# Kernel optimization log

Hardware: AMD Instinct MI355X
Metric: run time of the kernel (lower is better)

## Reference

```python
import jax, jax.numpy as jnp
import numpy as np

DEV_VDW, VDW_N, MAXV, MINV, DM_MIN = 0.2, 6.0, 0.0356, 0.0178, 0.5


def setup_inputs() -> dict:
    key = jax.random.key(0)
    ks = iter(jax.random.split(key, 64))
    B, N1, N2, D, L = 8, 128, 256, 128, 3
    f = jnp.float32
    nrm = lambda shape, s=0.05: jax.random.normal(next(ks), shape, f) * s
    ligand_h = jax.random.normal(next(ks), (B, N1, 54), f)
    target_h = jax.random.normal(next(ks), (B, N2, 54), f)
    def adj(n):
        a = (jax.random.uniform(next(ks), (B, n, n)) < 0.08).astype(f)
        a = jnp.maximum(a, jnp.swapaxes(a, 1, 2))
        return jnp.maximum(a, jnp.eye(n, dtype=f))
    ligand_adj = adj(N1)
    target_adj = adj(N2)
    interaction_indice = jax.random.uniform(next(ks), (B, 3, N1, N2), f)
    ligand_pos = jax.random.normal(next(ks), (B, N1, 3), f) * 2.0
    target_pos = jax.random.normal(next(ks), (B, N2, 3), f) * 4.0
    rotor = jax.random.uniform(next(ks), (B,), f) * 10.0
    ligand_vdw_radii = 1.2 + 0.8 * jax.random.uniform(next(ks), (B, N1), f)
    target_vdw_radii = 1.2 + 0.8 * jax.random.uniform(next(ks), (B, N2), f)
    return dict(
        ligand_h=ligand_h, ligand_adj=ligand_adj, target_h=target_h, target_adj=target_adj,
        interaction_indice=interaction_indice, ligand_pos=ligand_pos, target_pos=target_pos,
        rotor=rotor, ligand_vdw_radii=ligand_vdw_radii, target_vdw_radii=target_vdw_radii,
        ligand_valid=jnp.ones((B, N1), f), target_valid=jnp.ones((B, N2), f),
        ligand_non_metal=jnp.ones((B, N1), f), target_non_metal=jnp.ones((B, N2), f),
        emb_w=nrm((54, D)),
        gat_w=nrm((L, D, D)), gat_b=jnp.zeros((L, D), f), gat_att=nrm((L, D, D)),
        gat_gate_w=nrm((L, 2 * D, 1)), gat_gate_b=jnp.zeros((L, 1), f),
        int_wt_w=nrm((L, D, D)), int_wt_b=jnp.zeros((L, D), f),
        int_mt_w=nrm((L, D, D)), int_mt_b=jnp.zeros((L, D), f),
        gru_w_ih=nrm((L, 3 * D, D)), gru_w_hh=nrm((L, 3 * D, D)),
        gru_b_ih=jnp.zeros((L, 3 * D), f), gru_b_hh=jnp.zeros((L, 3 * D), f),
        A_w1=nrm((2 * D, D)), A_b1=jnp.zeros((D,), f), A_w2=nrm((D, 1)), A_b2=jnp.zeros((1,), f),
        B_w1=nrm((2 * D, D)), B_b1=jnp.zeros((D,), f), B_w2=nrm((D, 1)), B_b2=jnp.zeros((1,), f),
        hbond_coeff=jnp.array([1.0], f), hydrophobic_coeff=jnp.array([0.5], f),
        rotor_coeff=jnp.array([0.5], f),
    )


def reference(ligand_h, ligand_adj, target_h, target_adj, interaction_indice, ligand_pos,
              target_pos, rotor, ligand_vdw_radii, target_vdw_radii, ligand_valid,
              target_valid, ligand_non_metal, target_non_metal, emb_w, gat_w, gat_b,
              gat_att, gat_gate_w, gat_gate_b, int_wt_w, int_wt_b, int_mt_w, int_mt_b,
              gru_w_ih, gru_w_hh, gru_b_ih, gru_b_hh, A_w1, A_b1, A_w2, A_b2, B_w1, B_b1,
              B_w2, B_b2, hbond_coeff, hydrophobic_coeff, rotor_coeff):
    B, D, L = ligand_h.shape[0], emb_w.shape[1], gat_w.shape[0]

    def dist(lpos):
        diff = lpos[:, :, None, :] - target_pos[:, None, :, :]
        dm = jnp.sqrt((diff * diff).sum(-1) + 1e-10)
        return jnp.where(dm < DM_MIN, 1e10, dm)

    dm = dist(ligand_pos)

    def gat(x, adj, i):
        nt = x @ gat_w[i] + gat_b[i]                                   # [B,N,D]
        ea = jnp.einsum('bjl,bkl->bjk', nt @ gat_att[i], nt)
        ea = ea + jnp.swapaxes(ea, 1, 2)
        aw = jax.nn.softmax(jnp.where(adj > 1e-6, ea, -9e15), axis=-1) * adj
        out = jax.nn.relu(jnp.einsum('bij,bjd->bid', aw, nt))
        gate = jax.nn.sigmoid(jnp.concatenate([x, out], -1) @ gat_gate_w[i] + gat_gate_b[i])
        return gate * x + (1.0 - gate) * out

    lh = ligand_h @ emb_w
    th = target_h @ emb_w
    for i in range(L):
        lh = gat(lh, ligand_adj, i)
        th = gat(th, target_adj, i)

    adj12 = jax.lax.stop_gradient(dm)
    adj12 = jnp.where(adj12 > 5.0, 0.0, adj12)
    adj12 = jnp.where(adj12 > 1e-3, 1.0, 0.0)
    adj21 = jnp.swapaxes(adj12, 1, 2)

    def inter(a1, a2, ev, i):
        t1 = a1 @ int_wt_w[i] + int_wt_b[i]
        m2 = a2 @ int_mt_w[i] + int_mt_b[i]                            # [B,N2,D]
        t2 = (m2[:, None, :, :] * ev[..., None]).max(axis=2)           # [B,N1,D]
        msg = jax.nn.relu(t1 + t2)
        gi = msg @ gru_w_ih[i].T + gru_b_ih[i]
        gh = a1 @ gru_w_hh[i].T + gru_b_hh[i]
        i_r, i_z, i_n = jnp.split(gi, 3, -1)
        h_r, h_z, h_n = jnp.split(gh, 3, -1)
        r = jax.nn.sigmoid(i_r + h_r)
        z = jax.nn.sigmoid(i_z + h_z)
        n = jnp.tanh(i_n + r * h_n)
        return (1.0 - z) * n + z * a1

    for i in range(L):
        lh, th = inter(lh, th, adj12, i), inter(th, lh, adj21, i)

    N1, N2 = lh.shape[1], th.shape[1]
    h_cat = jnp.concatenate([
        jnp.broadcast_to(lh[:, :, None, :], (B, N1, N2, D)),
        jnp.broadcast_to(th[:, None, :, :], (B, N1, N2, D))], -1)      # [B,N1,N2,2D]

    A_raw = jax.nn.sigmoid(jax.nn.relu(h_cat @ A_w1 + A_b1) @ A_w2 + A_b2)[..., 0]
    B_raw = jnp.tanh(jax.nn.relu(h_cat @ B_w1 + B_b1) @ B_w2 + B_b2)[..., 0] * DEV_VDW
    dm0 = ligand_vdw_radii[:, :, None] + target_vdw_radii[:, None, :] + B_raw
    valid_pair = ligand_non_metal[:, :, None] * target_non_metal[:, None, :]
    A_vdw = A_raw * (MAXV - MINV) + MINV

    def energies_of(dm):
        dm0c = jnp.where(dm0 < 1e-4, 1.0, dm0)
        r6 = (dm0c / dm) ** VDW_N
        evdw = A_vdw * (jnp.minimum(r6 * r6 - 2.0 * r6, 100.0) * valid_pair)
        vdw_val = evdw.sum((1, 2))[:, None]
        dmd = dm - dm0
        def hb(Aind):
            r = jnp.clip(dmd * Aind / -0.7, 0.0, 1.0) * -(hbond_coeff[0] * hbond_coeff[0])
            return r.sum((1, 2))[:, None]
        hbond = hb(interaction_indice[:, 0])
        metal = hb(interaction_indice[:, 1])
        hp = jnp.clip((-dmd + 1.5) * interaction_indice[:, 2], 0.0, 1.0)
        hp = hp * -(hydrophobic_coeff[0] * hydrophobic_coeff[0])
        e = jnp.concatenate([vdw_val, hbond, metal, hp.sum((1, 2))[:, None]], -1)
        return e / (1.0 + rotor_coeff[0] * rotor_coeff[0] * rotor[:, None])

    energies = energies_of(dm)
    esum = lambda p: energies_of(dist(p)).sum()
    g = jax.grad(esum)(ligand_pos)
    der1 = (g.sum(1) ** 2).mean()
    der2 = -jax.grad(lambda p: jax.grad(esum)(p).sum())(ligand_pos).sum((1, 2)).mean()
    return energies, der1, der2
```

## Files before the change

kernel.cpp:

```cpp
#include <hip/hip_runtime.h>
#include <math.h>

#define BB 8
#define N1C 128
#define N2C 256
#define DC 128
#define NHC 54
#define ROWS_L 1024
#define ROWS_T 2048
#define ROWS_ALL 3072

__device__ __forceinline__ float wredSum(float v) {
#pragma unroll
  for (int o = 32; o > 0; o >>= 1) v += __shfl_down(v, o);
  return v;
}
__device__ float blockSum(float v) {
  __shared__ float red[9];
  v = wredSum(v);
  int lane = threadIdx.x & 63, wid = threadIdx.x >> 6;
  __syncthreads();
  if (lane == 0) red[wid] = v;
  __syncthreads();
  if (threadIdx.x == 0) {
    float s = 0.f;
    int nw = (blockDim.x + 63) >> 6;
    for (int i = 0; i < nw; ++i) s += red[i];
    red[8] = s;
  }
  __syncthreads();
  return red[8];
}

__global__ __launch_bounds__(256) void k_prep(
    const float* __restrict__ LP, const float* __restrict__ TP,
    float* __restrict__ AD, const float* __restrict__ LH,
    const float* __restrict__ TH, const float* __restrict__ EW,
    float* __restrict__ H0, const float* __restrict__ GWp,
    const float* __restrict__ GBp, const float* __restrict__ ATT,
    float* __restrict__ WA, float* __restrict__ bA,
    const float* __restrict__ IH, const float* __restrict__ HH,
    float* __restrict__ GIHT, float* __restrict__ GHHT) {
  int bid = blockIdx.x, tid = threadIdx.x;
  if (bid < 1024) {
    long idx = (long)bid * 256 + tid;
    int j = idx & (N2C - 1);
    long t = idx >> 8;
    int i = (int)(t & (N1C - 1));
    int b = (int)(t >> 7);
    float dx = LP[((long)b * N1C + i) * 3 + 0] - TP[((long)b * N2C + j) * 3 + 0];
    float dy = LP[((long)b * N1C + i) * 3 + 1] - TP[((long)b * N2C + j) * 3 + 1];
    float dz = LP[((long)b * N1C + i) * 3 + 2] - TP[((long)b * N2C + j) * 3 + 2];
    float d = sqrtf(dx * dx + dy * dy + dz * dz + 1e-10f);
    if (d < 0.5f) d = 1e10f;
    AD[idx] = (d <= 5.0f && d > 1e-3f) ? 1.f : 0.f;
  } else if (bid < 1024 + 384) {
    int r0 = (bid - 1024) * 8;
    __shared__ float xs[8][NHC];
    for (int t = tid; t < 8 * NHC; t += 256) {
      int rr = r0 + t / NHC, c = t % NHC;
      xs[t / NHC][c] = (rr < ROWS_L) ? LH[(long)rr * NHC + c]
                                     : TH[(long)(rr - ROWS_L) * NHC + c];
    }
    __syncthreads();
    int d = tid & 127, rb = (tid >> 7) * 4;
    float a[4] = {0.f, 0.f, 0.f, 0.f};
#pragma unroll 6
    for (int k = 0; k < NHC; ++k) {
      float wv = EW[(long)k * DC + d];
#pragma unroll
      for (int r = 0; r < 4; ++r) a[r] += xs[rb + r][k] * wv;
    }
#pragma unroll
    for (int r = 0; r < 4; ++r) H0[(long)(r0 + rb + r) * DC + d] = a[r];
  } else if (bid < 1024 + 384 + 99) {
    int q = bid - 1408;
    int l = q / 33, bx = q % 33;
    const float* Wl = GWp + (long)l * DC * DC;
    const float* Al = ATT + (long)l * DC * DC;
    if (bx == 32) {
      if (tid < 128) {
        float acc = 0.f;
#pragma unroll 8
        for (int m = 0; m < DC; ++m)
          acc += GBp[l * DC + m] * Al[(long)m * DC + tid];
        bA[l * DC + tid] = acc;
      }
    } else {
      __shared__ float xs2[4][DC];
      int r0 = bx * 4;
      for (int t = tid; t < 4 * DC; t += 256)
        xs2[t >> 7][t & 127] = Wl[(long)r0 * DC + t];
      __syncthreads();
      if (tid < 128) {
        int d = tid;
        float a0 = 0.f, a1 = 0.f, a2 = 0.f, a3 = 0.f;
#pragma unroll 8
        for (int m = 0; m < DC; ++m) {
          float av = Al[(long)m * DC + d];
          a0 += xs2[0][m] * av;
          a1 += xs2[1][m] * av;
          a2 += xs2[2][m] * av;
          a3 += xs2[3][m] * av;
        }
        float* out = WA + (long)l * DC * DC + (long)r0 * DC + d;
        out[0] = a0;
        out[DC] = a1;
        out[2 * DC] = a2;
        out[3 * DC] = a3;
      }
    }
  } else {
    long idx = (long)(bid - 1507) * 256 + tid;
    if (idx < 6L * 49152) {
      int a = (int)(idx / 49152);
      int rem = (int)(idx % 49152);
      int l = a >> 1, whh = a & 1;
      int c = rem / 384, rr = rem % 384;
      const float* src = (whh ? HH : IH) + (long)l * 49152;
      float* dst = (whh ? GHHT : GIHT) + (long)l * 49152;
      dst[(long)c * 384 + rr] = src[(long)rr * 128 + c];
    }
  }
}

__global__ __launch_bounds__(256) void k_lin2h(
    const float* __restrict__ X, const float* __restrict__ W1,
    const float* __restrict__ b1, const float* __restrict__ W2,
    const float* __restrict__ b2, float* __restrict__ Y1, float* __restrict__ Y2,
    int rpb, int trans) {
  int r0 = blockIdx.x * 4;
  __shared__ float xs_t[DC][4];
  int tid = threadIdx.x;
  for (int t = tid; t < 4 * DC; t += 256) {
    int r = t >> 7, c = t & 127;
    xs_t[c][r] = X[(long)(r0 + r) * DC + c];
  }
  __syncthreads();
  int h = tid >> 7, d = tid & 127;
  const float* W = h ? W2 : W1;
  const float* bp = h ? b2 : b1;
  float* Y = h ? Y2 : Y1;
  float a0 = 0.f, a1 = 0.f, a2 = 0.f, a3 = 0.f;
#pragma unroll 8
  for (int k = 0; k < DC; ++k) {
    float4 xv = *(const float4*)&xs_t[k][0];
    float wv = W[(long)k * DC + d];
    a0 = fmaf(xv.x, wv, a0);
    a1 = fmaf(xv.y, wv, a1);
    a2 = fmaf(xv.z, wv, a2);
    a3 = fmaf(xv.w, wv, a3);
  }
  float bv = bp ? bp[d] : 0.f;
  float v[4] = {a0 + bv, a1 + bv, a2 + bv, a3 + bv};
  if (!trans) {
#pragma unroll
    for (int r = 0; r < 4; ++r) Y[(long)(r0 + r) * DC + d] = v[r];
  } else {
    int b = r0 / rpb, rin = r0 - b * rpb;
#pragma unroll
    for (int r = 0; r < 4; ++r)
      Y[((long)b * DC + d) * rpb + rin + r] = v[r];
  }
}

__global__ __launch_bounds__(256) void k_ea2(const float* __restrict__ NTp,
                                             const float* __restrict__ E1p,
                                             const float* __restrict__ ADJL,
                                             const float* __restrict__ ADJT,
                                             float* __restrict__ EAL,
                                             float* __restrict__ EAT) {
  int id = blockIdx.x;
  int N, base, j0, k0, b;
  const float* ADJ;
  float* EA;
  if (id < 64) {
    b = id >> 3;
    int rem = id & 7;
    N = N1C;
    base = b * N1C;
    j0 = (rem >> 1) * 32;
    k0 = (rem & 1) * 64;
    ADJ = ADJL + (long)b * N1C * N1C;
    EA = EAL + (long)b * N1C * N1C;
  } else {
    int q = id - 64;
    b = q >> 5;
    int rem = q & 31;
    N = N2C;
    base = ROWS_L + b * N2C;
    j0 = (rem >> 2) * 32;
    k0 = (rem & 3) * 64;
    ADJ = ADJT + (long)b * N2C * N2C;
    EA = EAT + (long)b * N2C * N2C;
  }
  __shared__ float aj_e1[32][34], aj_nt[32][34];
  __shared__ float bk_e1[32][68], bk_nt[32][68];
  int tid = threadIdx.x, tx = tid & 15, ty = tid >> 4;
  float acc[2][4];
#pragma unroll
  for (int r = 0; r < 2; ++r)
#pragma unroll
    for (int c = 0; c < 4; ++c) acc[r][c] = 0.f;
  for (int kc = 0; kc < DC; kc += 32) {
    __syncthreads();
    for (int t = tid; t < 1024; t += 256) {
      int kk = t & 31, rr = t >> 5;
      aj_e1[kk][rr] = E1p[(long)(base + j0 + rr) * DC + kc + kk];
      aj_nt[kk][rr] = NTp[(long)(base + j0 + rr) * DC + kc + kk];
    }
    for (int t = tid; t < 2048; t += 256) {
      int kk = t & 31, cc = t >> 5;
      bk_e1[kk][cc] = E1p[(long)(base + k0 + cc) * DC + kc + kk];
      bk_nt[kk][cc] = NTp[(long)(base + k0 + cc) * DC + kc + kk];
    }
    __syncthreads();
#pragma unroll
    for (int kk = 0; kk < 32; ++kk) {
      float2 ae = *(const float2*)&aj_e1[kk][ty * 2];
      float2 an = *(const float2*)&aj_nt[kk][ty * 2];
      float4 bn = *(const float4*)&bk_nt[kk][tx * 4];
      float4 be = *(const float4*)&bk_e1[kk][tx * 4];
      acc[0][0] = fmaf(ae.x, bn.x, fmaf(an.x, be.x, acc[0][0]));
      acc[0][1] = fmaf(ae.x, bn.y, fmaf(an.x, be.y, acc[0][1]));
      acc[0][2] = fmaf(ae.x, bn.z, fmaf(an.x, be.z, acc[0][2]));
      acc[0][3] = fmaf(ae.x, bn.w, fmaf(an.x, be.w, acc[0][3]));
      acc[1][0] = fmaf(ae.y, bn.x, fmaf(an.y, be.x, acc[1][0]));
      acc[1][1] = fmaf(ae.y, bn.y, fmaf(an.y, be.y, acc[1][1]));
      acc[1][2] = fmaf(ae.y, bn.z, fmaf(an.y, be.z, acc[1][2]));
      acc[1][3] = fmaf(ae.y, bn.w, fmaf(an.y, be.w, acc[1][3]));
    }
  }
#pragma unroll
  for (int r = 0; r < 2; ++r) {
    long rowi = (long)(j0 + ty * 2 + r) * N + k0 + tx * 4;
    float4 ad = *(const float4*)&ADJ[rowi];
    float4 o;
    o.x = (ad.x > 1e-6f) ? acc[r][0] : -9e15f;
    o.y = (ad.y > 1e-6f) ? acc[r][1] : -9e15f;
    o.z = (ad.z > 1e-6f) ? acc[r][2] : -9e15f;
    o.w = (ad.w > 1e-6f) ? acc[r][3] : -9e15f;
    *(float4*)&EA[rowi] = o;
  }
}

__global__ __launch_bounds__(512) void k_smagg(
    const float* __restrict__ EAL, const float* __restrict__ EAT,
    const float* __restrict__ NTp, const float* __restrict__ Xp,
    const float* __restrict__ GW, const float* __restrict__ GB,
    float* __restrict__ Y) {
  int z = blockIdx.z;
  int N = z ? N2C : N1C;
  if (blockIdx.x * 8 >= N) return;
  int ls = z ? 8 : 7;
  int baseRow = z ? ROWS_L : 0;
  const float* EA = z ? EAT : EAL;
  int b = blockIdx.y, i0 = blockIdx.x * 8;
  __shared__ float ps[8][N2C + 4];
  __shared__ float col[32][DC + 4];
  __shared__ float red[8][2];
  int tid = threadIdx.x;
  const float* EAb = EA + (long)b * N * N + (long)i0 * N;
  for (int t = tid; t < 8 * N; t += 512)
    ps[t >> ls][t & (N - 1)] = EAb[t];
  __syncthreads();
  {
    int r = tid >> 6, l = tid & 63;
    float m = -INFINITY;
    for (int k = l; k < N; k += 64) m = fmaxf(m, ps[r][k]);
#pragma unroll
    for (int o = 32; o > 0; o >>= 1) m = fmaxf(m, __shfl_xor(m, o));
    float s = 0.f;
    for (int k = l; k < N; k += 64) {
      float p = expf(ps[r][k] - m);
      ps[r][k] = p;
      s += p;
    }
#pragma unroll
    for (int o = 32; o > 0; o >>= 1) s += __shfl_xor(s, o);
    float inv = 1.f / s;
    for (int k = l; k < N; k += 64) ps[r][k] *= inv;
  }
  int d = tid & 127, ro = tid >> 7;
  float acc[2] = {0.f, 0.f};
  const float* NTb = NTp + (long)(baseRow + b * N) * DC;
  for (int k0 = 0; k0 < N; k0 += 32) {
    __syncthreads();
    for (int t = tid; t < 32 * DC; t += 512)
      col[t >> 7][t & 127] = NTb[(long)(k0 + (t >> 7)) * DC + (t & 127)];
    __syncthreads();
#pragma unroll 8
    for (int kk = 0; kk < 32; ++kk) {
      float cv = col[kk][d];
      acc[0] = fmaf(ps[ro][k0 + kk], cv, acc[0]);
      acc[1] = fmaf(ps[ro + 4][k0 + kk], cv, acc[1]);
    }
  }
  float gwd = GW[d], gwo = GW[DC + d];
  float xv[2], ov[2], part[2];
#pragma unroll
  for (int q = 0; q < 2; ++q) {
    int r = ro + 4 * q;
    float o = fmaxf(acc[q], 0.f);
    ov[q] = o;
    float x = Xp[(long)(baseRow + b * N + i0 + r) * DC + d];
    xv[q] = x;
    part[q] = x * gwd + o * gwo;
  }
  int wid = tid >> 6;
#pragma unroll
  for (int q = 0; q < 2; ++q) {
    float v = wredSum(part[q]);
    if ((tid & 63) == 0) red[wid][q] = v;
  }
  __syncthreads();
  float gb = GB[0];
#pragma unroll
  for (int q = 0; q < 2; ++q) {
    int r = ro + 4 * q;
    float s = red[2 * ro][q] + red[2 * ro + 1][q];
    float g = 1.f / (1.f + expf(-(s + gb)));
    Y[(long)(baseRow + b * N + i0 + r) * DC + d] = g * xv[q] + (1.f - g) * ov[q];
  }
}

__global__ __launch_bounds__(256) void k_msg2v(const float* __restrict__ T1,
                                               const float* __restrict__ M2,
                                               const float* __restrict__ EV,
                                               float* __restrict__ MSG) {
  int z = blockIdx.z, b = blockIdx.y;
  int Ni = z ? N2C : N1C, Nj = z ? N1C : N2C;
  if (blockIdx.x * 8 >= Ni) return;
  int t1off = z ? ROWS_L : 0, m2off = z ? 0 : ROWS_L;
  long ev_is = z ? 1L : (long)N2C, ev_js = z ? (long)N2C : 1L;
  int i0 = blockIdx.x * 8;
  __shared__ float m2s[32][DC + 4];
  __shared__ float evs[8][36];
  int dgrp = threadIdx.x & 31, row = threadIdx.x >> 5;
  int d0 = dgrp * 4;
  float a0 = -INFINITY, a1 = -INFINITY, a2 = -INFINITY, a3 = -INFINITY;
  const float* M2b = M2 + (long)(m2off + b * Nj) * DC;
  const float* EVb = EV + (long)b * (N1C * N2C);
  for (int j0 = 0; j0 < Nj; j0 += 32) {
    __syncthreads();
    for (int t = threadIdx.x; t < 32 * DC; t += 256)
      m2s[t >> 7][t & 127] = M2b[(long)(j0 + (t >> 7)) * DC + (t & 127)];
    for (int t = threadIdx.x; t < 256; t += 256)
      evs[t >> 5][t & 31] =
          EVb[(long)(i0 + (t >> 5)) * ev_is + (long)(j0 + (t & 31)) * ev_js];
    __syncthreads();
#pragma unroll 8
    for (int jj = 0; jj < 32; ++jj) {
      float4 m4 = *(const float4*)&m2s[jj][d0];
      float e = evs[row][jj];
      a0 = fmaxf(a0, m4.x * e);
      a1 = fmaxf(a1, m4.y * e);
      a2 = fmaxf(a2, m4.z * e);
      a3 = fmaxf(a3, m4.w * e);
    }
  }
  long grow = t1off + (long)b * Ni + i0 + row;
  float4 t4 = *(const float4*)&T1[grow * DC + d0];
  float4 o;
  o.x = fmaxf(t4.x + a0, 0.f);
  o.y = fmaxf(t4.y + a1, 0.f);
  o.z = fmaxf(t4.z + a2, 0.f);
  o.w = fmaxf(t4.w + a3, 0.f);
  *(float4*)&MSG[grow * DC + d0] = o;
}

__global__ __launch_bounds__(384) void k_gruf(
    const float* __restrict__ MSGp, const float* __restrict__ Hp,
    const float* __restrict__ WihT, const float* __restrict__ WhhT,
    const float* __restrict__ bih, const float* __restrict__ bhh,
    float* __restrict__ Y) {
  const int D = DC;
  int r0 = blockIdx.x * 4;
  __shared__ float xs_t[DC][4], hs_t[DC][4];
  __shared__ float gis[4][384], ghs[4][384];
  int tid = threadIdx.x;
  for (int t = tid; t < 4 * DC; t += 384) {
    int r = t >> 7, c = t & 127;
    xs_t[c][r] = MSGp[(long)(r0 + r) * D + c];
    hs_t[c][r] = Hp[(long)(r0 + r) * D + c];
  }
  __syncthreads();
  int dd = tid;
  float ai[4] = {0.f, 0.f, 0.f, 0.f}, ah[4] = {0.f, 0.f, 0.f, 0.f};
#pragma unroll 8
  for (int k = 0; k < DC; ++k) {
    float4 xv = *reinterpret_cast<const float4*>(&xs_t[k][0]);
    float4 hv = *reinterpret_cast<const float4*>(&hs_t[k][0]);
    float wi = WihT[(long)k * 384 + dd];
    float wh = WhhT[(long)k * 384 + dd];
    ai[0] = fmaf(xv.x, wi, ai[0]);
    ai[1] = fmaf(xv.y, wi, ai[1]);
    ai[2] = fmaf(xv.z, wi, ai[2]);
    ai[3] = fmaf(xv.w, wi, ai[3]);
    ah[0] = fmaf(hv.x, wh, ah[0]);
    ah[1] = fmaf(hv.y, wh, ah[1]);
    ah[2] = fmaf(hv.z, wh, ah[2]);
    ah[3] = fmaf(hv.w, wh, ah[3]);
  }
  float bi = bih[dd], bh = bhh[dd];
#pragma unroll
  for (int r = 0; r < 4; ++r) {
    gis[r][dd] = ai[r] + bi;
    ghs[r][dd] = ah[r] + bh;
  }
  __syncthreads();
  for (int t = tid; t < 4 * DC; t += 384) {
    int r = t >> 7, d = t & 127;
    float ir = gis[r][d], iz = gis[r][d + 128], inn = gis[r][d + 256];
    float hr = ghs[r][d], hz = ghs[r][d + 128], hn = ghs[r][d + 256];
    float rg = 1.f / (1.f + expf(-(ir + hr)));
    float zg = 1.f / (1.f + expf(-(iz + hz)));
    float ng = tanhf(inn + rg * hn);
    Y[(long)(r0 + r) * D + d] = (1.f - zg) * ng + zg * hs_t[d][r];
  }
}

__global__ __launch_bounds__(256) void k_pair(
    const float* __restrict__ UA, const float* __restrict__ VAT,
    const float* __restrict__ UB, const float* __restrict__ VBT,
    const float* __restrict__ AW2, const float* __restrict__ AB2,
    const float* __restrict__ BW2, const float* __restrict__ BB2,
    const float* __restrict__ LP, const float* __restrict__ TP,
    const float* __restrict__ LVDW, const float* __restrict__ TVDW,
    const float* __restrict__ LNM, const float* __restrict__ TNM,
    const float* __restrict__ II, const float* __restrict__ HBC,
    const float* __restrict__ HPC, float* __restrict__ PART) {
  const int D = DC, N1 = N1C, N2 = N2C;
  int i = blockIdx.x, b = blockIdx.y, j = threadIdx.x;
  __shared__ float ua[128], ub[128], wa2[128], wb2[128];
  if (j < 128) {
    long rb = ((long)b * N1 + i) * D + j;
    ua[j] = UA[rb];
    ub[j] = UB[rb];
    wa2[j] = AW2[j];
    wb2[j] = BW2[j];
  }
  __syncthreads();
  const float* vat = VAT + (long)b * D * N2;
  const float* vbt = VBT + (long)b * D * N2;
  float dotA = 0.f, dotB = 0.f;
#pragma unroll 8
  for (int d = 0; d < D; ++d) {
    dotA += fmaxf(ua[d] + vat[(long)d * N2 + j], 0.f) * wa2[d];
    dotB += fmaxf(ub[d] + vbt[(long)d * N2 + j], 0.f) * wb2[d];
  }
  float A_raw = 1.f / (1.f + expf(-(dotA + AB2[0])));
  float A_vdw = A_raw * (0.0356f - 0.0178f) + 0.0178f;
  float B_raw = tanhf(dotB + BB2[0]) * 0.2f;

  float lx = LP[((long)b * N1 + i) * 3 + 0];
  float ly = LP[((long)b * N1 + i) * 3 + 1];
  float lz = LP[((long)b * N1 + i) * 3 + 2];
  float tx = TP[((long)b * N2 + j) * 3 + 0];
  float ty = TP[((long)b * N2 + j) * 3 + 1];
  float tz = TP[((long)b * N2 + j) * 3 + 2];
  float dx = lx - tx, dy = ly - ty, dz = lz - tz;
  float s2 = dx * dx + dy * dy + dz * dz + 1e-10f;
  float draw = sqrtf(s2);
  bool clamped = draw < 0.5f;
  float dmv = clamped ? 1e10f : draw;

  float dm0 = LVDW[b * N1 + i] + TVDW[b * N2 + j] + B_raw;
  float dm0c = (dm0 < 1e-4f) ? 1.f : dm0;
  float valid = LNM[b * N1 + i] * TNM[b * N2 + j];

  float rr = dm0c / dmv;
  float r2 = rr * rr, r6 = r2 * r2 * r2;
  float fv = r6 * r6 - 2.f * r6;
  float evdw = A_vdw * (fminf(fv, 100.f) * valid);

  float dmd = dmv - dm0;
  long ii0 = ((long)b * 3) * N1 * N2 + (long)i * N2 + j;
  float I0 = II[ii0];
  float I1 = II[ii0 + (long)N1 * N2];
  float I2 = II[ii0 + 2L * N1 * N2];
  float hb2 = HBC[0] * HBC[0], hp2 = HPC[0] * HPC[0];
  float u0 = dmd * I0 / (-0.7f);
  float u1 = dmd * I1 / (-0.7f);
  float vv = (1.5f - dmd) * I2;
  float ehb = fminf(fmaxf(u0, 0.f), 1.f) * (-hb2);
  float emt = fminf(fmaxf(u1, 0.f), 1.f) * (-hb2);
  float ehp = fminf(fmaxf(vv, 0.f), 1.f) * (-hp2);

  float gx = 0.f, gy = 0.f, gz = 0.f, d2t = 0.f;
  if (!clamped) {
    float Ep = 0.f, Epp = 0.f;
    if (fv < 100.f) {
      float c = A_vdw * valid;
      Ep += c * (-12.f) * r6 * (r6 - 1.f) / draw;
      Epp += c * r6 * (156.f * r6 - 84.f) / s2;
    }
    if (u0 > 0.f && u0 < 1.f) Ep += hb2 * I0 * (1.f / 0.7f);
    if (u1 > 0.f && u1 < 1.f) Ep += hb2 * I1 * (1.f / 0.7f);
    if (vv > 0.f && vv < 1.f) Ep += hp2 * I2;
    float invd = 1.f / draw;
    gx = Ep * dx * invd;
    gy = Ep * dy * invd;
    gz = Ep * dz * invd;
    float T = dx + dy + dz;
    float tt = T * T / s2;
    d2t = Epp * tt + Ep * (3.f - tt) * invd;
  }

  float o0 = blockSum(evdw);
  float o1 = blockSum(ehb);
  float o2 = blockSum(emt);
  float o3 = blockSum(ehp);
  float o4 = blockSum(gx);
  float o5 = blockSum(gy);
  float o6 = blockSum(gz);
  float o7 = blockSum(d2t);
  if (j == 0) {
    float* p = PART + ((long)b * N1 + i) * 8;
    p[0] = o0; p[1] = o1; p[2] = o2; p[3] = o3;
    p[4] = o4; p[5] = o5; p[6] = o6; p[7] = o7;
  }
}

__global__ void k_final(const float* __restrict__ PART, const float* __restrict__ ROT,
                        const float* __restrict__ RC, float* __restrict__ OUT) {
  const int N1 = N1C;
  __shared__ float s[8][8];
  int t = threadIdx.x;
  if (t < 64) {
    int b = t >> 3, k1 = t & 7;
    float acc = 0.f;
    for (int i = 0; i < N1; ++i) acc += PART[((long)b * N1 + i) * 8 + k1];
    s[b][k1] = acc;
  }
  __syncthreads();
  if (t == 0) {
    float rcc = RC[0] * RC[0];
    float der1 = 0.f, der2 = 0.f;
    for (int b = 0; b < 8; ++b) {
      float w = 1.f / (1.f + rcc * ROT[b]);
      OUT[b * 4 + 0] = s[b][0] * w;
      OUT[b * 4 + 1] = s[b][1] * w;
      OUT[b * 4 + 2] = s[b][2] * w;
      OUT[b * 4 + 3] = s[b][3] * w;
      for (int c = 0; c < 3; ++c) {
        float S = s[b][4 + c] * w;
        der1 += S * S;
      }
      der2 += s[b][7] * w;
    }
    OUT[32] = der1 / 24.f;
    OUT[33] = -der2 / 8.f;
  }
}

extern "C" void kernel_launch(void* const* d_in, const int* in_sizes, int n_in,
                              void* d_out, int out_size, void* d_ws, size_t ws_size,
                              hipStream_t stream) {
  (void)in_sizes; (void)n_in; (void)out_size; (void)ws_size;
  const int D = DC;

  const float* ligand_h   = (const float*)d_in[0];
  const float* ligand_adj = (const float*)d_in[1];
  const float* target_h   = (const float*)d_in[2];
  const float* target_adj = (const float*)d_in[3];
  const float* inter_ind  = (const float*)d_in[4];
  const float* ligand_pos = (const float*)d_in[5];
  const float* target_pos = (const float*)d_in[6];
  const float* rotor      = (const float*)d_in[7];
  const float* lvdw       = (const float*)d_in[8];
  const float* tvdw       = (const float*)d_in[9];
  const float* lnm        = (const float*)d_in[12];
  const float* tnm        = (const float*)d_in[13];
  const float* emb_w      = (const float*)d_in[14];
  const float* gat_w      = (const float*)d_in[15];
  const float* gat_b      = (const float*)d_in[16];
  const float* gat_att    = (const float*)d_in[17];
  const float* gat_gate_w = (const float*)d_in[18];
  const float* gat_gate_b = (const float*)d_in[19];
  const float* int_wt_w   = (const float*)d_in[20];
  const float* int_wt_b   = (const float*)d_in[21];
  const float* int_mt_w   = (const float*)d_in[22];
  const float* int_mt_b   = (const float*)d_in[23];
  const float* gru_w_ih   = (const float*)d_in[24];
  const float* gru_w_hh   = (const float*)d_in[25];
  const float* gru_b_ih   = (const float*)d_in[26];
  const float* gru_b_hh   = (const float*)d_in[27];
  const float* A_w1       = (const float*)d_in[28];
  const float* A_b1       = (const float*)d_in[29];
  const float* A_w2       = (const float*)d_in[30];
  const float* A_b2       = (const float*)d_in[31];
  const float* B_w1       = (const float*)d_in[32];
  const float* B_b1       = (const float*)d_in[33];
  const float* B_w2       = (const float*)d_in[34];
  const float* B_b2       = (const float*)d_in[35];
  const float* hb_c       = (const float*)d_in[36];
  const float* hp_c       = (const float*)d_in[37];
  const float* rc_c       = (const float*)d_in[38];

  float* w = (float*)d_ws;
  auto take = [&](size_t n) { float* p = w; w += n; return p; };
  float* H0    = take((size_t)ROWS_ALL * DC);
  float* H1    = take((size_t)ROWS_ALL * DC);
  float* NT    = take((size_t)ROWS_ALL * DC);
  float* E1    = take((size_t)ROWS_ALL * DC);
  float* EAL   = take((size_t)BB * N1C * N1C);
  float* EAT   = take((size_t)BB * N2C * N2C);
  float* ADJ12 = take((size_t)BB * N1C * N2C);
  float* WA    = take((size_t)3 * DC * DC);
  float* bA    = take((size_t)3 * DC);
  float* GIHT  = take((size_t)3 * DC * 384);
  float* GHHT  = take((size_t)3 * DC * 384);
  float* PART  = take((size_t)BB * N1C * 8);
  float* T1  = NT;
  float* M2  = E1;
  float* MSG = EAT;
  float* UA  = EAL;
  float* UB  = EAT;
  float* VAT = NT;
  float* VBT = E1;

  k_prep<<<2659, 256, 0, stream>>>(ligand_pos, target_pos, ADJ12, ligand_h,
                                   target_h, emb_w, H0, gat_w, gat_b, gat_att,
                                   WA, bA, gru_w_ih, gru_w_hh, GIHT, GHHT);

  float *cur = H0, *alt = H1;

  for (int l = 0; l < 3; ++l) {
    k_lin2h<<<ROWS_ALL / 4, 256, 0, stream>>>(
        cur, gat_w + (size_t)l * D * D, gat_b + l * D, WA + (size_t)l * D * D,
        bA + l * D, NT, E1, 1, 0);
    k_ea2<<<320, 256, 0, stream>>>(NT, E1, ligand_adj, target_adj, EAL, EAT);
    k_smagg<<<dim3(N2C / 8, BB, 2), 512, 0, stream>>>(
        EAL, EAT, NT, cur, gat_gate_w + l * 2 * D, gat_gate_b + l, alt);
    float* t = cur; cur = alt; alt = t;
  }

  for (int l = 0; l < 3; ++l) {
    k_lin2h<<<ROWS_ALL / 4, 256, 0, stream>>>(
        cur, int_wt_w + (size_t)l * D * D, int_wt_b + l * D,
        int_mt_w + (size_t)l * D * D, int_mt_b + l * D, T1, M2, 1, 0);
    k_msg2v<<<dim3(32, 8, 2), 256, 0, stream>>>(T1, M2, ADJ12, MSG);
    k_gruf<<<ROWS_ALL / 4, 384, 0, stream>>>(MSG, cur, GIHT + (size_t)l * D * 384,
                                             GHHT + (size_t)l * D * 384,
                                             gru_b_ih + l * 384,
                                             gru_b_hh + l * 384, alt);
    float* t = cur; cur = alt; alt = t;
  }

  k_lin2h<<<ROWS_L / 4, 256, 0, stream>>>(cur, A_w1, A_b1, B_w1, B_b1, UA, UB,
                                          1, 0);
  k_lin2h<<<ROWS_T / 4, 256, 0, stream>>>(cur + (size_t)ROWS_L * DC,
                                          A_w1 + D * D, nullptr, B_w1 + D * D,
                                          nullptr, VAT, VBT, N2C, 1);

  k_pair<<<dim3(N1C, BB), 256, 0, stream>>>(UA, VAT, UB, VBT, A_w2, A_b2, B_w2,
                                            B_b2, ligand_pos, target_pos, lvdw,
                                            tvdw, lnm, tnm, inter_ind, hb_c,
                                            hp_c, PART);

  k_final<<<1, 256, 0, stream>>>(PART, rotor, rc_c, (float*)d_out);
}
```

Before: 351.2 us.

## Process more rows per block in smagg, GRU and pair kernels for reuse

Three kernels now do more rows per block so each staged operand is reused more. k_smagg handles 16 rows per block instead of 8, uses a 32-lane group per row, vectorises the column reads as float4 and reduces the gate within each group. k_gruf computes 8 rows per block so each weight load feeds 8 FMAs instead of 4. k_pair handles two ligand atoms per block, sharing the VAT/VBT column loads across both. The trade-offs are fewer blocks (lower occupancy and parallelism) and more registers per thread.

```diff
diff --git a/kernel.cpp b/kernel.cpp
--- a/kernel.cpp
+++ b/kernel.cpp
@@ -244,45 +244,45 @@
   }
 }
 
-__global__ __launch_bounds__(512) void k_smagg(
+__global__ __launch_bounds__(512) void k_smagg3(
     const float* __restrict__ EAL, const float* __restrict__ EAT,
     const float* __restrict__ NTp, const float* __restrict__ Xp,
     const float* __restrict__ GW, const float* __restrict__ GB,
     float* __restrict__ Y) {
   int z = blockIdx.z;
   int N = z ? N2C : N1C;
-  if (blockIdx.x * 8 >= N) return;
+  if (blockIdx.x * 16 >= N) return;
   int ls = z ? 8 : 7;
   int baseRow = z ? ROWS_L : 0;
   const float* EA = z ? EAT : EAL;
-  int b = blockIdx.y, i0 = blockIdx.x * 8;
-  __shared__ float ps[8][N2C + 4];
+  int b = blockIdx.y, i0 = blockIdx.x * 16;
+  __shared__ float ps[16][N2C + 4];
   __shared__ float col[32][DC + 4];
-  __shared__ float red[8][2];
+  __shared__ float red[16];
   int tid = threadIdx.x;
   const float* EAb = EA + (long)b * N * N + (long)i0 * N;
-  for (int t = tid; t < 8 * N; t += 512)
+  for (int t = tid; t < 16 * N; t += 512)
     ps[t >> ls][t & (N - 1)] = EAb[t];
   __syncthreads();
+  int r = tid >> 5, l = tid & 31;
   {
-    int r = tid >> 6, l = tid & 63;
     float m = -INFINITY;
-    for (int k = l; k < N; k += 64) m = fmaxf(m, ps[r][k]);
-#pragma unroll
-    for (int o = 32; o > 0; o >>= 1) m = fmaxf(m, __shfl_xor(m, o));
+    for (int k = l; k < N; k += 32) m = fmaxf(m, ps[r][k]);
+#pragma unroll
+    for (int o = 16; o > 0; o >>= 1) m = fmaxf(m, __shfl_xor(m, o));
     float s = 0.f;
-    for (int k = l; k < N; k += 64) {
+    for (int k = l; k < N; k += 32) {
       float p = expf(ps[r][k] - m);
       ps[r][k] = p;
       s += p;
     }
 #pragma unroll
-    for (int o = 32; o > 0; o >>= 1) s += __shfl_xor(s, o);
+    for (int o = 16; o > 0; o >>= 1) s += __shfl_xor(s, o);
     float inv = 1.f / s;
-    for (int k = l; k < N; k += 64) ps[r][k] *= inv;
-  }
-  int d = tid & 127, ro = tid >> 7;
-  float acc[2] = {0.f, 0.f};
+    for (int k = l; k < N; k += 32) ps[r][k] *= inv;
+  }
+  int d0 = l * 4;
+  float a0 = 0.f, a1 = 0.f, a2 = 0.f, a3 = 0.f;
   const float* NTb = NTp + (long)(baseRow + b * N) * DC;
   for (int k0 = 0; k0 < N; k0 += 32) {
     __syncthreads();
@@ -291,37 +291,32 @@
     __syncthreads();
 #pragma unroll 8
     for (int kk = 0; kk < 32; ++kk) {
-      float cv = col[kk][d];
-      acc[0] = fmaf(ps[ro][k0 + kk], cv, acc[0]);
-      acc[1] = fmaf(ps[ro + 4][k0 + kk], cv, acc[1]);
-    }
-  }
-  float gwd = GW[d], gwo = GW[DC + d];
-  float xv[2], ov[2], part[2];
-#pragma unroll
-  for (int q = 0; q < 2; ++q) {
-    int r = ro + 4 * q;
-    float o = fmaxf(acc[q], 0.f);
-    ov[q] = o;
-    float x = Xp[(long)(baseRow + b * N + i0 + r) * DC + d];
-    xv[q] = x;
-    part[q] = x * gwd + o * gwo;
-  }
-  int wid = tid >> 6;
-#pragma unroll
-  for (int q = 0; q < 2; ++q) {
-    float v = wredSum(part[q]);
-    if ((tid & 63) == 0) red[wid][q] = v;
-  }
-  __syncthreads();
-  float gb = GB[0];
-#pragma unroll
-  for (int q = 0; q < 2; ++q) {
-    int r = ro + 4 * q;
-    float s = red[2 * ro][q] + red[2 * ro + 1][q];
-    float g = 1.f / (1.f + expf(-(s + gb)));
-    Y[(long)(baseRow + b * N + i0 + r) * DC + d] = g * xv[q] + (1.f - g) * ov[q];
-  }
+      float4 c4 = *(const float4*)&col[kk][d0];
+      float p = ps[r][k0 + kk];
+      a0 = fmaf(p, c4.x, a0);
+      a1 = fmaf(p, c4.y, a1);
+      a2 = fmaf(p, c4.z, a2);
+      a3 = fmaf(p, c4.w, a3);
+    }
+  }
+  float4 gwd = *(const float4*)&GW[d0];
+  float4 gwo = *(const float4*)&GW[DC + d0];
+  float4 x4 = *(const float4*)&Xp[(long)(baseRow + b * N + i0 + r) * DC + d0];
+  float o0 = fmaxf(a0, 0.f), o1 = fmaxf(a1, 0.f);
+  float o2 = fmaxf(a2, 0.f), o3 = fmaxf(a3, 0.f);
+  float part = x4.x * gwd.x + o0 * gwo.x + x4.y * gwd.y + o1 * gwo.y +
+               x4.z * gwd.z + o2 * gwo.z + x4.w * gwd.w + o3 * gwo.w;
+#pragma unroll
+  for (int o = 16; o > 0; o >>= 1) part += __shfl_xor(part, o);
+  if (l == 0) red[r] = part;
+  __syncthreads();
+  float g = 1.f / (1.f + expf(-(red[r] + GB[0])));
+  float4 y;
+  y.x = g * x4.x + (1.f - g) * o0;
+  y.y = g * x4.y + (1.f - g) * o1;
+  y.z = g * x4.z + (1.f - g) * o2;
+  y.w = g * x4.w + (1.f - g) * o3;
+  *(float4*)&Y[(long)(baseRow + b * N + i0 + r) * DC + d0] = y;
 }
 
 __global__ __launch_bounds__(256) void k_msg2v(const float* __restrict__ T1,
@@ -375,41 +370,53 @@
     const float* __restrict__ bih, const float* __restrict__ bhh,
     float* __restrict__ Y) {
   const int D = DC;
-  int r0 = blockIdx.x * 4;
-  __shared__ float xs_t[DC][4], hs_t[DC][4];
-  __shared__ float gis[4][384], ghs[4][384];
+  int r0 = blockIdx.x * 8;
+  __shared__ float xs_t[DC][8], hs_t[DC][8];
+  __shared__ float gis[8][384], ghs[8][384];
   int tid = threadIdx.x;
-  for (int t = tid; t < 4 * DC; t += 384) {
+  for (int t = tid; t < 8 * DC; t += 384) {
     int r = t >> 7, c = t & 127;
     xs_t[c][r] = MSGp[(long)(r0 + r) * D + c];
     hs_t[c][r] = Hp[(long)(r0 + r) * D + c];
   }
   __syncthreads();
   int dd = tid;
-  float ai[4] = {0.f, 0.f, 0.f, 0.f}, ah[4] = {0.f, 0.f, 0.f, 0.f};
-#pragma unroll 8
+  float ai[8], ah[8];
+#pragma unroll
+  for (int r = 0; r < 8; ++r) { ai[r] = 0.f; ah[r] = 0.f; }
+#pragma unroll 4
   for (int k = 0; k < DC; ++k) {
-    float4 xv = *reinterpret_cast<const float4*>(&xs_t[k][0]);
-    float4 hv = *reinterpret_cast<const float4*>(&hs_t[k][0]);
+    float4 xv0 = *(const float4*)&xs_t[k][0];
+    float4 xv1 = *(const float4*)&xs_t[k][4];
+    float4 hv0 = *(const float4*)&hs_t[k][0];
+    float4 hv1 = *(const float4*)&hs_t[k][4];
     float wi = WihT[(long)k * 384 + dd];
     float wh = WhhT[(long)k * 384 + dd];
-    ai[0] = fmaf(xv.x, wi, ai[0]);
-    ai[1] = fmaf(xv.y, wi, ai[1]);
-    ai[2] = fmaf(xv.z, wi, ai[2]);
-    ai[3] = fmaf(xv.w, wi, ai[3]);
-    ah[0] = fmaf(hv.x, wh, ah[0]);
-    ah[1] = fmaf(hv.y, wh, ah[1]);
-    ah[2] = fmaf(hv.z, wh, ah[2]);
-    ah[3] = fmaf(hv.w, wh, ah[3]);
+    ai[0] = fmaf(xv0.x, wi, ai[0]);
+    ai[1] = fmaf(xv0.y, wi, ai[1]);
+    ai[2] = fmaf(xv0.z, wi, ai[2]);
+    ai[3] = fmaf(xv0.w, wi, ai[3]);
+    ai[4] = fmaf(xv1.x, wi, ai[4]);
+    ai[5] = fmaf(xv1.y, wi, ai[5]);
+    ai[6] = fmaf(xv1.z, wi, ai[6]);
+    ai[7] = fmaf(xv1.w, wi, ai[7]);
+    ah[0] = fmaf(hv0.x, wh, ah[0]);
+    ah[1] = fmaf(hv0.y, wh, ah[1]);
+    ah[2] = fmaf(hv0.z, wh, ah[2]);
+    ah[3] = fmaf(hv0.w, wh, ah[3]);
+    ah[4] = fmaf(hv1.x, wh, ah[4]);
+    ah[5] = fmaf(hv1.y, wh, ah[5]);
+    ah[6] = fmaf(hv1.z, wh, ah[6]);
+    ah[7] = fmaf(hv1.w, wh, ah[7]);
   }
   float bi = bih[dd], bh = bhh[dd];
 #pragma unroll
-  for (int r = 0; r < 4; ++r) {
+  for (int r = 0; r < 8; ++r) {
     gis[r][dd] = ai[r] + bi;
     ghs[r][dd] = ah[r] + bh;
   }
   __syncthreads();
-  for (int t = tid; t < 4 * DC; t += 384) {
+  for (int t = tid; t < 8 * DC; t += 384) {
     int r = t >> 7, d = t & 127;
     float ir = gis[r][d], iz = gis[r][d + 128], inn = gis[r][d + 256];
     float hr = ghs[r][d], hz = ghs[r][d + 128], hn = ghs[r][d + 256];
@@ -431,94 +438,115 @@
     const float* __restrict__ II, const float* __restrict__ HBC,
     const float* __restrict__ HPC, float* __restrict__ PART) {
   const int D = DC, N1 = N1C, N2 = N2C;
-  int i = blockIdx.x, b = blockIdx.y, j = threadIdx.x;
-  __shared__ float ua[128], ub[128], wa2[128], wb2[128];
+  int i0 = blockIdx.x * 2, b = blockIdx.y, j = threadIdx.x;
+  __shared__ float ua[2][128], ub[2][128], wa2[128], wb2[128];
   if (j < 128) {
-    long rb = ((long)b * N1 + i) * D + j;
-    ua[j] = UA[rb];
-    ub[j] = UB[rb];
+    long rb = ((long)b * N1 + i0) * D + j;
+    ua[0][j] = UA[rb];
+    ub[0][j] = UB[rb];
     wa2[j] = AW2[j];
     wb2[j] = BW2[j];
+  } else {
+    int jj = j - 128;
+    long rb = ((long)b * N1 + i0 + 1) * D + jj;
+    ua[1][jj] = UA[rb];
+    ub[1][jj] = UB[rb];
   }
   __syncthreads();
   const float* vat = VAT + (long)b * D * N2;
   const float* vbt = VBT + (long)b * D * N2;
-  float dotA = 0.f, dotB = 0.f;
-#pragma unroll 8
+  float dotA[2] = {0.f, 0.f}, dotB[2] = {0.f, 0.f};
+#pragma unroll 4
   for (int d = 0; d < D; ++d) {
-    dotA += fmaxf(ua[d] + vat[(long)d * N2 + j], 0.f) * wa2[d];
-    dotB += fmaxf(ub[d] + vbt[(long)d * N2 + j], 0.f) * wb2[d];
-  }
-  float A_raw = 1.f / (1.f + expf(-(dotA + AB2[0])));
-  float A_vdw = A_raw * (0.0356f - 0.0178f) + 0.0178f;
-  float B_raw = tanhf(dotB + BB2[0]) * 0.2f;
-
-  float lx = LP[((long)b * N1 + i) * 3 + 0];
-  float ly = LP[((long)b * N1 + i) * 3 + 1];
-  float lz = LP[((long)b * N1 + i) * 3 + 2];
+    float va = vat[(long)d * N2 + j];
+    float vb = vbt[(long)d * N2 + j];
+    dotA[0] += fmaxf(ua[0][d] + va, 0.f) * wa2[d];
+    dotA[1] += fmaxf(ua[1][d] + va, 0.f) * wa2[d];
+    dotB[0] += fmaxf(ub[0][d] + vb, 0.f) * wb2[d];
+    dotB[1] += fmaxf(ub[1][d] + vb, 0.f) * wb2[d];
+  }
+  float hb2 = HBC[0] * HBC[0], hp2 = HPC[0] * HPC[0];
   float tx = TP[((long)b * N2 + j) * 3 + 0];
   float ty = TP[((long)b * N2 + j) * 3 + 1];
   float tz = TP[((long)b * N2 + j) * 3 + 2];
-  float dx = lx - tx, dy = ly - ty, dz = lz - tz;
-  float s2 = dx * dx + dy * dy + dz * dz + 1e-10f;
-  float draw = sqrtf(s2);
-  bool clamped = draw < 0.5f;
-  float dmv = clamped ? 1e10f : draw;
-
-  float dm0 = LVDW[b * N1 + i] + TVDW[b * N2 + j] + B_raw;
-  float dm0c = (dm0 < 1e-4f) ? 1.f : dm0;
-  float valid = LNM[b * N1 + i] * TNM[b * N2 + j];
-
-  float rr = dm0c / dmv;
-  float r2 = rr * rr, r6 = r2 * r2 * r2;
-  float fv = r6 * r6 - 2.f * r6;
-  float evdw = A_vdw * (fminf(fv, 100.f) * valid);
-
-  float dmd = dmv - dm0;
-  long ii0 = ((long)b * 3) * N1 * N2 + (long)i * N2 + j;
-  float I0 = II[ii0];
-  float I1 = II[ii0 + (long)N1 * N2];
-  float I2 = II[ii0 + 2L * N1 * N2];
-  float hb2 = HBC[0] * HBC[0], hp2 = HPC[0] * HPC[0];
-  float u0 = dmd * I0 / (-0.7f);
-  float u1 = dmd * I1 / (-0.7f);
-  float vv = (1.5f - dmd) * I2;
-  float ehb = fminf(fmaxf(u0, 0.f), 1.f) * (-hb2);
-  float emt = fminf(fmaxf(u1, 0.f), 1.f) * (-hb2);
-  float ehp = fminf(fmaxf(vv, 0.f), 1.f) * (-hp2);
-
-  float gx = 0.f, gy = 0.f, gz = 0.f, d2t = 0.f;
-  if (!clamped) {
-    float Ep = 0.f, Epp = 0.f;
-    if (fv < 100.f) {
-      float c = A_vdw * valid;
-      Ep += c * (-12.f) * r6 * (r6 - 1.f) / draw;
-      Epp += c * r6 * (156.f * r6 - 84.f) / s2;
-    }
-    if (u0 > 0.f && u0 < 1.f) Ep += hb2 * I0 * (1.f / 0.7f);
-    if (u1 > 0.f && u1 < 1.f) Ep += hb2 * I1 * (1.f / 0.7f);
-    if (vv > 0.f && vv < 1.f) Ep += hp2 * I2;
-    float invd = 1.f / draw;
-    gx = Ep * dx * invd;
-    gy = Ep * dy * invd;
-    gz = Ep * dz * invd;
-    float T = dx + dy + dz;
-    float tt = T * T / s2;
-    d2t = Epp * tt + Ep * (3.f - tt) * invd;
-  }
-
-  float o0 = blockSum(evdw);
-  float o1 = blockSum(ehb);
-  float o2 = blockSum(emt);
-  float o3 = blockSum(ehp);
-  float o4 = blockSum(gx);
-  float o5 = blockSum(gy);
-  float o6 = blockSum(gz);
-  float o7 = blockSum(d2t);
-  if (j == 0) {
-    float* p = PART + ((long)b * N1 + i) * 8;
-    p[0] = o0; p[1] = o1; p[2] = o2; p[3] = o3;
-    p[4] = o4; p[5] = o5; p[6] = o6; p[7] = o7;
+  float tvd = TVDW[b * N2 + j];
+  float tnm = TNM[b * N2 + j];
+  float res[2][8];
+#pragma unroll
+  for (int ii = 0; ii < 2; ++ii) {
+    int i = i0 + ii;
+    float A_raw = 1.f / (1.f + expf(-(dotA[ii] + AB2[0])));
+    float A_vdw = A_raw * (0.0356f - 0.0178f) + 0.0178f;
+    float B_raw = tanhf(dotB[ii] + BB2[0]) * 0.2f;
+
+    float lx = LP[((long)b * N1 + i) * 3 + 0];
+    float ly = LP[((long)b * N1 + i) * 3 + 1];
+    float lz = LP[((long)b * N1 + i) * 3 + 2];
+    float dx = lx - tx, dy = ly - ty, dz = lz - tz;
+    float s2 = dx * dx + dy * dy + dz * dz + 1e-10f;
+    float draw = sqrtf(s2);
+    bool clamped = draw < 0.5f;
+    float dmv = clamped ? 1e10f : draw;
+
+    float dm0 = LVDW[b * N1 + i] + tvd + B_raw;
+    float dm0c = (dm0 < 1e-4f) ? 1.f : dm0;
+    float valid = LNM[b * N1 + i] * tnm;
+
+    float rr = dm0c / dmv;
+    float r2 = rr * rr, r6 = r2 * r2 * r2;
+    float fv = r6 * r6 - 2.f * r6;
+    float evdw = A_vdw * (fminf(fv, 100.f) * valid);
+
+    float dmd = dmv - dm0;
+    long ii0x = ((long)b * 3) * N1 * N2 + (long)i * N2 + j;
+    float I0 = II[ii0x];
+    float I1 = II[ii0x + (long)N1 * N2];
+    float I2 = II[ii0x + 2L * N1 * N2];
+    float u0 = dmd * I0 / (-0.7f);
+    float u1 = dmd * I1 / (-0.7f);
+    float vv = (1.5f - dmd) * I2;
+    float ehb = fminf(fmaxf(u0, 0.f), 1.f) * (-hb2);
+    float emt = fminf(fmaxf(u1, 0.f), 1.f) * (-hb2);
+    float ehp = fminf(fmaxf(vv, 0.f), 1.f) * (-hp2);
+
+    float gx = 0.f, gy = 0.f, gz = 0.f, d2t = 0.f;
+    if (!clamped) {
+      float Ep = 0.f, Epp = 0.f;
+      if (fv < 100.f) {
+        float c = A_vdw * valid;
+        Ep += c * (-12.f) * r6 * (r6 - 1.f) / draw;
+        Epp += c * r6 * (156.f * r6 - 84.f) / s2;
+      }
+      if (u0 > 0.f && u0 < 1.f) Ep += hb2 * I0 * (1.f / 0.7f);
+      if (u1 > 0.f && u1 < 1.f) Ep += hb2 * I1 * (1.f / 0.7f);
+      if (vv > 0.f && vv < 1.f) Ep += hp2 * I2;
+      float invd = 1.f / draw;
+      gx = Ep * dx * invd;
+      gy = Ep * dy * invd;
+      gz = Ep * dz * invd;
+      float T = dx + dy + dz;
+      float tt = T * T / s2;
+      d2t = Epp * tt + Ep * (3.f - tt) * invd;
+    }
+    res[ii][0] = evdw;
+    res[ii][1] = ehb;
+    res[ii][2] = emt;
+    res[ii][3] = ehp;
+    res[ii][4] = gx;
+    res[ii][5] = gy;
+    res[ii][6] = gz;
+    res[ii][7] = d2t;
+  }
+#pragma unroll
+  for (int ii = 0; ii < 2; ++ii) {
+    float o[8];
+#pragma unroll
+    for (int q = 0; q < 8; ++q) o[q] = blockSum(res[ii][q]);
+    if (j == 0) {
+      float* p = PART + ((long)b * N1 + i0 + ii) * 8;
+#pragma unroll
+      for (int q = 0; q < 8; ++q) p[q] = o[q];
+    }
   }
 }
 
@@ -631,7 +659,7 @@
         cur, gat_w + (size_t)l * D * D, gat_b + l * D, WA + (size_t)l * D * D,
         bA + l * D, NT, E1, 1, 0);
     k_ea2<<<320, 256, 0, stream>>>(NT, E1, ligand_adj, target_adj, EAL, EAT);
-    k_smagg<<<dim3(N2C / 8, BB, 2), 512, 0, stream>>>(
+    k_smagg3<<<dim3(N2C / 16, BB, 2), 512, 0, stream>>>(
         EAL, EAT, NT, cur, gat_gate_w + l * 2 * D, gat_gate_b + l, alt);
     float* t = cur; cur = alt; alt = t;
   }
@@ -641,7 +669,7 @@
         cur, int_wt_w + (size_t)l * D * D, int_wt_b + l * D,
         int_mt_w + (size_t)l * D * D, int_mt_b + l * D, T1, M2, 1, 0);
     k_msg2v<<<dim3(32, 8, 2), 256, 0, stream>>>(T1, M2, ADJ12, MSG);
-    k_gruf<<<ROWS_ALL / 4, 384, 0, stream>>>(MSG, cur, GIHT + (size_t)l * D * 384,
+    k_gruf<<<ROWS_ALL / 8, 384, 0, stream>>>(MSG, cur, GIHT + (size_t)l * D * 384,
                                              GHHT + (size_t)l * D * 384,
                                              gru_b_ih + l * 384,
                                              gru_b_hh + l * 384, alt);
@@ -654,10 +682,11 @@
                                           A_w1 + D * D, nullptr, B_w1 + D * D,
                                           nullptr, VAT, VBT, N2C, 1);
 
-  k_pair<<<dim3(N1C, BB), 256, 0, stream>>>(UA, VAT, UB, VBT, A_w2, A_b2, B_w2,
-                                            B_b2, ligand_pos, target_pos, lvdw,
-                                            tvdw, lnm, tnm, inter_ind, hb_c,
-                                            hp_c, PART);
+  k_pair<<<dim3(N1C / 2, BB), 256, 0, stream>>>(UA, VAT, UB, VBT, A_w2, A_b2,
+                                                B_w2, B_b2, ligand_pos,
+                                                target_pos, lvdw, tvdw, lnm,
+                                                tnm, inter_ind, hb_c, hp_c,
+                                                PART);
 
   k_final<<<1, 256, 0, stream>>>(PART, rotor, rc_c, (float*)d_out);
 }
```

Result: slower. 447.9 us (+27.5%).
